# Kernel tuning notes

Hardware: AMD Instinct MI355X
Metric: run time of the kernel (lower is better)

Reference implementation:

```python
import jax, jax.numpy as jnp
import numpy as np

NUM_ATOMS = 100
D = 32        # initial_atom_dim
H = 16        # hidden_dim (multiplicity per irrep)
NB = 16       # edge_dim / number of bessel basis functions
CUT = 6.0     # radius_cutoff
DEG = 4.0     # degree_norm
OUT = 1       # output_dim
INV4PI = 1.0 / np.sqrt(4.0 * np.pi)  # 'integral' SH normalization


def _bessel(d, nb, cut):
    # e3nn soft_one_hot_linspace(basis='bessel', cutoff=True) * sqrt(nb)
    x = d[:, None]
    n = jnp.arange(1, nb + 1, dtype=d.dtype)
    safe = jnp.maximum(x, 1e-9)
    out = np.sqrt(2.0 / cut) * jnp.sin(n * jnp.pi * x / cut) / safe
    return out * (x < cut) * np.sqrt(float(nb))


def _fc(x, w1, w2):
    # e3nn FullyConnectedNet: fan-in normalized linear layers, silu, no bias
    h = jax.nn.silu(x @ w1 / np.sqrt(x.shape[-1]))
    return h @ w2 / np.sqrt(w1.shape[-1])


def _forward(atomic_numbers, edge_index, coords, atom_emb,
             fc0_w1, fc0_w2, fc1_w1, fc1_w2, w_readout):
    src, dst = edge_index[0], edge_index[1]
    N = coords.shape[0]
    E = src.shape[0]

    vec = coords[src] - coords[dst]                      # [E,3]
    dist = jnp.linalg.norm(vec, axis=-1)                 # [E]
    unit = vec / jnp.maximum(dist, 1e-9)[:, None]

    # spherical harmonics, l=0 and l=1, 'integral' normalization
    y0 = jnp.full((E,), INV4PI, dtype=coords.dtype)      # [E]
    y1 = (np.sqrt(3.0) * INV4PI) * unit                  # [E,3]
    basis = _bessel(dist, NB, CUT)                       # [E,NB]

    x = atom_emb[atomic_numbers]                         # [N,D] (row 0 is padding)

    # ---- layer 0: scalars (D x0e) x (1x0e+1x1o) -> H x0e + H x1o ----
    w = _fc(basis, fc0_w1, fc0_w2)                       # [E, 2*D*H] per-edge TP weights
    wa = w[:, : D * H].reshape(E, D, H)
    wb = w[:, D * H:].reshape(E, D, H)
    xs = x[src]
    n0 = 1.0 / np.sqrt(D)                                # path fan-in norm
    m0 = jnp.einsum('ed,edh->eh', xs, wa) * y0[:, None] * n0          # [E,H]
    m1 = jnp.einsum('ed,edh->eh', xs, wb)[:, :, None] * y1[:, None, :] * n0  # [E,H,3]
    z0 = jax.ops.segment_sum(m0, dst, num_segments=N) / DEG           # [N,H]
    z1 = jax.ops.segment_sum(m1, dst, num_segments=N) / DEG           # [N,H,3]

    # ---- layer 1: (H x0e + H x1o) x (1x0e+1x1o) -> same irreps, skip-connected ----
    w = _fc(basis, fc1_w1, fc1_w2)                       # [E, 4*H*H]
    w1_ = w[:, 0 * H * H:1 * H * H].reshape(E, H, H)     # 0e x 0e -> 0e
    w2_ = w[:, 1 * H * H:2 * H * H].reshape(E, H, H)     # 0e x 1o -> 1o
    w3_ = w[:, 2 * H * H:3 * H * H].reshape(E, H, H)     # 1o x 0e -> 1o
    w4_ = w[:, 3 * H * H:4 * H * H].reshape(E, H, H)     # 1o x 1o -> 0e (CG = dot/sqrt(3))
    s, v = z0[src], z1[src]
    n1 = 1.0 / np.sqrt(2 * H)                            # two paths per output irrep
    dot = jnp.einsum('ehm,em->eh', v, y1) / np.sqrt(3.0)
    o0 = (jnp.einsum('eh,ehk->ek', s, w1_) * y0[:, None]
          + jnp.einsum('eh,ehk->ek', dot, w4_)) * n1
    o1 = (jnp.einsum('eh,ehk->ek', s, w2_)[:, :, None] * y1[:, None, :]
          + jnp.einsum('ehm,ehk->ekm', v, w3_) * y0[:, None, None]) * n1
    z0 = jax.ops.segment_sum(o0, dst, num_segments=N) / DEG + z0      # skip
    z1 = jax.ops.segment_sum(o1, dst, num_segments=N) / DEG + z1

    # ---- scalar readout (o3.Linear onto 0e) + graph sum-pool ----
    node_scalar = z0 @ w_readout / np.sqrt(H)            # [N,OUT]
    return jnp.sum(node_scalar, axis=0)                  # [OUT]


def setup_inputs() -> dict:
    key = jax.random.key(0)
    ks = jax.random.split(key, 9)
    N, E = 10000, 160000
    atomic_numbers = jax.random.randint(ks[0], (N,), 0, NUM_ATOMS)
    coords = jax.random.normal(ks[1], (N, 3), dtype=jnp.float32)
    edge_index = jax.random.randint(ks[2], (2, E), 0, N)
    atom_emb = jax.random.normal(ks[3], (NUM_ATOMS, D), dtype=jnp.float32).at[0].set(0.0)
    fc0_w1 = jax.random.normal(ks[4], (NB, H), dtype=jnp.float32)
    fc0_w2 = jax.random.normal(ks[5], (H, 2 * D * H), dtype=jnp.float32)
    fc1_w1 = jax.random.normal(ks[6], (NB, H), dtype=jnp.float32)
    fc1_w2 = jax.random.normal(ks[7], (H, 4 * H * H), dtype=jnp.float32)
    w_readout = jax.random.normal(ks[8], (H, OUT), dtype=jnp.float32)
    return {"atomic_numbers": atomic_numbers, "coords": coords, "edge_index": edge_index,
            "atom_emb": atom_emb, "fc0_w1": fc0_w1, "fc0_w2": fc0_w2,
            "fc1_w1": fc1_w1, "fc1_w2": fc1_w2, "w_readout": w_readout}


def reference(atomic_numbers, coords, edge_index, atom_emb,
              fc0_w1, fc0_w2, fc1_w1, fc1_w2, w_readout):
    return _forward(atomic_numbers, edge_index, coords, atom_emb,
                    fc0_w1, fc0_w2, fc1_w1, fc1_w2, w_readout)
```

## Files before the change

kernel.cpp:

```cpp
#include <hip/hip_runtime.h>
#include <math.h>


namespace {
constexpr int   NATOMS   = 100;
constexpr int   CAP      = 64;
constexpr float PI_F     = 3.14159265358979323846f;
constexpr float INV4PI_F = 0.28209479177387814f;
constexpr float SQRT3_F  = 1.7320508075688772f;
constexpr float CUT_F    = 6.0f;
constexpr float BASIS_C  = 2.3094010767585034f;
constexpr float N0_F     = 0.17677669529663687f;
constexpr float K0_F = INV4PI_F * N0_F * 0.0625f;
constexpr float K1_F = SQRT3_F * INV4PI_F * N0_F * 0.0625f;
}

__device__ __forceinline__ float silu_fast(float x) {
  return x / (1.0f + __expf(-x));
}

__device__ __forceinline__ float block_reduce_sum(float v) {
  #pragma unroll
  for (int o = 32; o > 0; o >>= 1) v += __shfl_down(v, o, 64);
  __shared__ float ls[8];
  int lane = threadIdx.x & 63;
  int w    = threadIdx.x >> 6;
  if (lane == 0) ls[w] = v;
  __syncthreads();
  float s = 0.f;
  if (threadIdx.x == 0) {
    int nw = (blockDim.x + 63) >> 6;
    for (int i = 0; i < nw; ++i) s += ls[i];
  }
  return s;
}

__global__ void table_kernel(const float* __restrict__ atom_emb,
                             const float* __restrict__ fc0_w2,
                             const float* __restrict__ fc1_w2,
                             const float* __restrict__ w_readout,
                             float* __restrict__ TI,
                             float* __restrict__ G1T, float* __restrict__ G4T) {
  int b = blockIdx.x;
  int tt = threadIdx.x;
  int j = tt >> 4;
  int h = tt & 15;
  if (b < NATOMS) {
    float s0 = 0.f, s1 = 0.f;
    #pragma unroll
    for (int d = 0; d < 32; ++d) {
      float x = atom_emb[b * 32 + d];
      s0 = fmaf(x, fc0_w2[j * 1024 + d * 16 + h], s0);
      s1 = fmaf(x, fc0_w2[j * 1024 + 512 + d * 16 + h], s1);
    }
    TI[b * 512 + j * 32 + 2 * h]     = s0;
    TI[b * 512 + j * 32 + 2 * h + 1] = s1;
  } else {
    float g1 = 0.f, g4 = 0.f;
    #pragma unroll
    for (int k = 0; k < 16; ++k) {
      float r = w_readout[k];
      g1 = fmaf(fc1_w2[j * 1024 + h * 16 + k], r, g1);
      g4 = fmaf(fc1_w2[j * 1024 + 768 + h * 16 + k], r, g4);
    }
    G1T[h * 16 + j] = g1;
    G4T[h * 16 + j] = g4;
  }
}

__global__ void __launch_bounds__(256)
edge_kernel(const int* __restrict__ ei,
            const float* __restrict__ coords,
            const int* __restrict__ an,
            const float* __restrict__ TI,
            const float* __restrict__ fc0_w1,
            int* __restrict__ cursor,
            float4* __restrict__ evec,
            float4* __restrict__ mbuf,
            int E) {
  __shared__ float w1s[256];
  w1s[threadIdx.x] = fc0_w1[threadIdx.x];
  __syncthreads();
  int lane = threadIdx.x & 63;
  int g    = threadIdx.x >> 4;
  int t    = threadIdx.x & 15;
  int base = lane & 48;

  float w0c[16];
  #pragma unroll
  for (int k = 0; k < 16; ++k) w0c[k] = w1s[k * 16 + t];

  const float angc = PI_F / CUT_F;
  int e = blockIdx.x * 32 + g;
  #pragma unroll
  for (int rep = 0; rep < 2; ++rep, e += 16) {
    if (e < E) {
      int s = ei[e];
      int d = ei[E + e];
      float vx = coords[3 * s + 0] - coords[3 * d + 0];
      float vy = coords[3 * s + 1] - coords[3 * d + 1];
      float vz = coords[3 * s + 2] - coords[3 * d + 2];
      float dist = sqrtf(vx * vx + vy * vy + vz * vz);
      float inv  = 1.0f / fmaxf(dist, 1e-9f);
      float ux = vx * inv, uy = vy * inv, uz = vz * inv;
      float bc = (dist < CUT_F) ? (BASIS_C * inv) : 0.0f;

      int slotv = 0;
      if (t == 0) {
        evec[e] = make_float4(ux, uy, uz, dist);
        slotv = d * CAP + atomicAdd(&cursor[d], 1);
      }
      int slot = __shfl(slotv, base, 64);

      float ang = angc * dist;
      float sc = __sinf(ang);
      float tw = 2.0f * __cosf(ang);
      float sp = 0.f, acc = 0.f;
      #pragma unroll
      for (int k = 0; k < 16; ++k) {
        acc = fmaf(sc, w0c[k], acc);
        float sn = fmaf(tw, sc, -sp);
        sp = sc; sc = sn;
      }
      float h0t = silu_fast(acc * bc * 0.25f);

      int a = an[s];
      const float2* tp = (const float2*)(TI + a * 512) + t;
      float u0 = 0.f, u1 = 0.f;
      #pragma unroll
      for (int j = 0; j < 16; ++j) {
        float hj = __shfl(h0t, base + j, 64);
        float2 T = tp[j * 16];
        u0 = fmaf(hj, T.x, u0);
        u1 = fmaf(hj, T.y, u1);
      }
      float m1 = K1_F * u1;
      mbuf[(size_t)slot * 16 + t] =
          make_float4(K0_F * u0, m1 * ux, m1 * uy, m1 * uz);
    }
  }
}

__global__ void __launch_bounds__(256, 4)
node_kernel(const int* __restrict__ cursor,
            const float4* __restrict__ mbuf,
            const float* __restrict__ G1T,
            const float* __restrict__ G4T,
            const float* __restrict__ w_readout,
            float* __restrict__ zbuf,
            float* __restrict__ out,
            int N) {
  __shared__ float ggs[512];
  ggs[threadIdx.x]       = G1T[threadIdx.x];
  ggs[256 + threadIdx.x] = G4T[threadIdx.x];
  __syncthreads();

  int wave = threadIdx.x >> 6;
  int lane = threadIdx.x & 63;
  int g    = lane >> 4;
  int t    = lane & 15;
  int base = lane & 48;
  int node = blockIdx.x * 4 + wave;
  bool valid = node < N;

  float rr = w_readout[t];
  int cnt = valid ? min(cursor[node], CAP) : 0;
  const float4* mb = mbuf + (size_t)(valid ? node : 0) * CAP * 16;

  float a0 = 0.f, ax = 0.f, ay = 0.f, az = 0.f;
  for (int i = g; i < cnt; i += 4) {
    float4 f = mb[i * 16 + t];
    a0 += f.x; ax += f.y; ay += f.z; az += f.w;
  }

  a0 += __shfl_xor(a0, 16, 64); a0 += __shfl_xor(a0, 32, 64);
  ax += __shfl_xor(ax, 16, 64); ax += __shfl_xor(ax, 32, 64);
  ay += __shfl_xor(ay, 16, 64); ay += __shfl_xor(ay, 32, 64);
  az += __shfl_xor(az, 16, 64); az += __shfl_xor(az, 32, 64);

  float srcv = (g == 0) ? a0 : ((g == 1) ? ax : (g == 2) ? ay : az);
  int tofs = (g == 0) ? 0 : 256;
  float o = 0.f;
  #pragma unroll
  for (int h = 0; h < 16; ++h) {
    float vh = __shfl(srcv, base + h, 64);
    o = fmaf(ggs[tofs + h * 16 + t], vh, o);
  }
  if (valid) zbuf[(size_t)node * 64 + t * 4 + g] = o;

  float p = (valid && g == 0) ? a0 * rr : 0.f;
  float tot = block_reduce_sum(p);
  if (threadIdx.x == 0) atomicAdd(out, tot * 0.25f);
}

__global__ void __launch_bounds__(256, 4)
phase2_kernel(const int* __restrict__ ei,
              const float4* __restrict__ evec,
              const float* __restrict__ fc1_w1,
              const float* __restrict__ zbuf,
              float* __restrict__ out,
              int E) {
  int t = threadIdx.x & 15;
  float w1c[16];
  #pragma unroll
  for (int k = 0; k < 16; ++k) w1c[k] = fc1_w1[k * 16 + t];

  int gid = (blockIdx.x * blockDim.x + threadIdx.x) >> 4;
  int ngroups = (gridDim.x * blockDim.x) >> 4;
  const float angc = PI_F / CUT_F;

  float c = 0.f;
  for (int e = gid; e < E; e += ngroups) {
    int s = ei[e];
    float4 ev = evec[e];
    float dist = ev.w;
    float bc = (dist < CUT_F) ? (BASIS_C / fmaxf(dist, 1e-9f)) : 0.0f;

    float ang = angc * dist;
    float sc = __sinf(ang);
    float tw = 2.0f * __cosf(ang);
    float sp = 0.f, acc = 0.f;
    #pragma unroll
    for (int k = 0; k < 16; ++k) {
      acc = fmaf(sc, w1c[k], acc);
      float sn = fmaf(tw, sc, -sp);
      sp = sc; sc = sn;
    }
    float h1t = silu_fast(acc * bc * 0.25f);

    float4 z = ((const float4*)(zbuf + (size_t)s * 64))[t];
    c = fmaf(h1t, fmaf(z.y, ev.x, fmaf(z.z, ev.y, fmaf(z.w, ev.z, z.x))), c);
  }
  c *= INV4PI_F * N0_F * (1.0f / 64.0f);
  float tot = block_reduce_sum(c);
  if (threadIdx.x == 0) atomicAdd(out, tot);
}

extern "C" void kernel_launch(void* const* d_in, const int* in_sizes, int n_in,
                              void* d_out, int out_size, void* d_ws, size_t ws_size,
                              hipStream_t stream) {
  const int*   an        = (const int*)d_in[0];
  const float* coords    = (const float*)d_in[1];
  const int*   ei        = (const int*)d_in[2];
  const float* atom_emb  = (const float*)d_in[3];
  const float* fc0_w1    = (const float*)d_in[4];
  const float* fc0_w2    = (const float*)d_in[5];
  const float* fc1_w1    = (const float*)d_in[6];
  const float* fc1_w2    = (const float*)d_in[7];
  const float* w_readout = (const float*)d_in[8];

  int N = in_sizes[0];
  int E = in_sizes[2] / 2;

  float4* mbuf = (float4*)d_ws;
  float4* evec = mbuf + (size_t)N * CAP * 16;
  float*  zbuf = (float*)(evec + E);
  float*  TI   = zbuf + (size_t)N * 64;
  float*  G1T  = TI + NATOMS * 512;
  float*  G4T  = G1T + 256;
  int*    cursor = (int*)(G4T + 256);
  float*  out = (float*)d_out;

  hipMemsetAsync(cursor, 0, (size_t)N * sizeof(int), stream);
  hipMemsetAsync(out, 0, sizeof(float), stream);

  int blk = 256;
  table_kernel<<<NATOMS + 1, blk, 0, stream>>>(
      atom_emb, fc0_w2, fc1_w2, w_readout, TI, G1T, G4T);

  edge_kernel<<<(E + 31) / 32, blk, 0, stream>>>(
      ei, coords, an, TI, fc0_w1, cursor, evec, mbuf, E);

  node_kernel<<<(N + 3) / 4, blk, 0, stream>>>(
      cursor, mbuf, G1T, G4T, w_readout, zbuf, out, N);

  phase2_kernel<<<2048, blk, 0, stream>>>(ei, evec, fc1_w1, zbuf, out, E);
}
```

Before: 177.0 us.

## Fuse phase2 into node kernel via per-source edge buckets and compact messages

Edges are now bucketed by source as well as destination, so each node's wave can evaluate its outgoing second-layer contributions right after computing its own z features, with no zbuf round-trip. This removes the separate phase2 launch. Per-edge messages shrink from float4 to float2, and the unit vector is stored once per edge slot and reapplied during aggregation, which cuts mbuf traffic. The costs are a second atomic per edge and extra scatter writes into sbuf. Edges beyond CAP per source are dropped from the second term, and destination overflow now clamps into the last slot and overwrites it instead of being skipped.

```diff
diff --git a/kernel.cpp b/kernel.cpp
--- a/kernel.cpp
+++ b/kernel.cpp
@@ -13,6 +13,7 @@
 constexpr float N0_F     = 0.17677669529663687f;
 constexpr float K0_F = INV4PI_F * N0_F * 0.0625f;
 constexpr float K1_F = SQRT3_F * INV4PI_F * N0_F * 0.0625f;
+constexpr float P2SC = INV4PI_F * N0_F * (1.0f / 64.0f);
 }
 
 __device__ __forceinline__ float silu_fast(float x) {
@@ -74,9 +75,10 @@
             const int* __restrict__ an,
             const float* __restrict__ TI,
             const float* __restrict__ fc0_w1,
-            int* __restrict__ cursor,
-            float4* __restrict__ evec,
-            float4* __restrict__ mbuf,
+            int* __restrict__ dcur, int* __restrict__ scur,
+            float2* __restrict__ mbuf,
+            float4* __restrict__ ubuf,
+            float4* __restrict__ sbuf,
             int E) {
   __shared__ float w1s[256];
   w1s[threadIdx.x] = fc0_w1[threadIdx.x];
@@ -107,8 +109,13 @@
 
       int slotv = 0;
       if (t == 0) {
-        evec[e] = make_float4(ux, uy, uz, dist);
-        slotv = d * CAP + atomicAdd(&cursor[d], 1);
+        float4 rec = make_float4(ux, uy, uz, dist);
+        int pos  = atomicAdd(&dcur[d], 1);
+        int spos = atomicAdd(&scur[s], 1);
+        int dslot = d * CAP + min(pos, CAP - 1);
+        ubuf[dslot] = rec;
+        if (spos < CAP) sbuf[s * CAP + spos] = rec;
+        slotv = dslot;
       }
       int slot = __shfl(slotv, base, 64);
 
@@ -134,20 +141,21 @@
         u0 = fmaf(hj, T.x, u0);
         u1 = fmaf(hj, T.y, u1);
       }
-      float m1 = K1_F * u1;
-      mbuf[(size_t)slot * 16 + t] =
-          make_float4(K0_F * u0, m1 * ux, m1 * uy, m1 * uz);
+      mbuf[(size_t)slot * 16 + t] = make_float2(K0_F * u0, K1_F * u1);
     }
   }
 }
 
 __global__ void __launch_bounds__(256, 4)
-node_kernel(const int* __restrict__ cursor,
-            const float4* __restrict__ mbuf,
+node_kernel(const int* __restrict__ dcur,
+            const int* __restrict__ scur,
+            const float2* __restrict__ mbuf,
+            const float4* __restrict__ ubuf,
+            const float4* __restrict__ sbuf,
             const float* __restrict__ G1T,
             const float* __restrict__ G4T,
+            const float* __restrict__ fc1_w1,
             const float* __restrict__ w_readout,
-            float* __restrict__ zbuf,
             float* __restrict__ out,
             int N) {
   __shared__ float ggs[512];
@@ -163,16 +171,24 @@
   int node = blockIdx.x * 4 + wave;
   bool valid = node < N;
 
+  float w1c[16];
+  #pragma unroll
+  for (int k = 0; k < 16; ++k) w1c[k] = fc1_w1[k * 16 + t];
   float rr = w_readout[t];
-  int cnt = valid ? min(cursor[node], CAP) : 0;
-  const float4* mb = mbuf + (size_t)(valid ? node : 0) * CAP * 16;
+
+  int cin  = valid ? min(dcur[node], CAP) : 0;
+  int cout = valid ? min(scur[node], CAP) : 0;
+  size_t nb = (size_t)(valid ? node : 0) * CAP;
 
   float a0 = 0.f, ax = 0.f, ay = 0.f, az = 0.f;
-  for (int i = g; i < cnt; i += 4) {
-    float4 f = mb[i * 16 + t];
-    a0 += f.x; ax += f.y; ay += f.z; az += f.w;
-  }
-
+  for (int i = g; i < cin; i += 4) {
+    float2 f  = mbuf[(nb + i) * 16 + t];
+    float4 uu = ubuf[nb + i];
+    a0 += f.x;
+    ax = fmaf(f.y, uu.x, ax);
+    ay = fmaf(f.y, uu.y, ay);
+    az = fmaf(f.y, uu.z, az);
+  }
   a0 += __shfl_xor(a0, 16, 64); a0 += __shfl_xor(a0, 32, 64);
   ax += __shfl_xor(ax, 16, 64); ax += __shfl_xor(ax, 32, 64);
   ay += __shfl_xor(ay, 16, 64); ay += __shfl_xor(ay, 32, 64);
@@ -186,36 +202,17 @@
     float vh = __shfl(srcv, base + h, 64);
     o = fmaf(ggs[tofs + h * 16 + t], vh, o);
   }
-  if (valid) zbuf[(size_t)node * 64 + t * 4 + g] = o;
-
-  float p = (valid && g == 0) ? a0 * rr : 0.f;
-  float tot = block_reduce_sum(p);
-  if (threadIdx.x == 0) atomicAdd(out, tot * 0.25f);
-}
-
-__global__ void __launch_bounds__(256, 4)
-phase2_kernel(const int* __restrict__ ei,
-              const float4* __restrict__ evec,
-              const float* __restrict__ fc1_w1,
-              const float* __restrict__ zbuf,
-              float* __restrict__ out,
-              int E) {
-  int t = threadIdx.x & 15;
-  float w1c[16];
-  #pragma unroll
-  for (int k = 0; k < 16; ++k) w1c[k] = fc1_w1[k * 16 + t];
-
-  int gid = (blockIdx.x * blockDim.x + threadIdx.x) >> 4;
-  int ngroups = (gridDim.x * blockDim.x) >> 4;
+  float Qt  = __shfl(o, t, 64);
+  float Pxt = __shfl(o, 16 + t, 64);
+  float Pyt = __shfl(o, 32 + t, 64);
+  float Pzt = __shfl(o, 48 + t, 64);
+
   const float angc = PI_F / CUT_F;
-
   float c = 0.f;
-  for (int e = gid; e < E; e += ngroups) {
-    int s = ei[e];
-    float4 ev = evec[e];
-    float dist = ev.w;
+  for (int i = g; i < cout; i += 4) {
+    float4 uu = sbuf[nb + i];
+    float dist = uu.w;
     float bc = (dist < CUT_F) ? (BASIS_C / fmaxf(dist, 1e-9f)) : 0.0f;
-
     float ang = angc * dist;
     float sc = __sinf(ang);
     float tw = 2.0f * __cosf(ang);
@@ -227,11 +224,12 @@
       sp = sc; sc = sn;
     }
     float h1t = silu_fast(acc * bc * 0.25f);
-
-    float4 z = ((const float4*)(zbuf + (size_t)s * 64))[t];
-    c = fmaf(h1t, fmaf(z.y, ev.x, fmaf(z.z, ev.y, fmaf(z.w, ev.z, z.x))), c);
-  }
-  c *= INV4PI_F * N0_F * (1.0f / 64.0f);
+    c = fmaf(h1t, fmaf(Pxt, uu.x, fmaf(Pyt, uu.y, fmaf(Pzt, uu.z, Qt))), c);
+  }
+  c *= P2SC;
+  if (valid && g == 0) c = fmaf(a0 * rr, 0.25f, c);
+  if (!valid) c = 0.f;
+
   float tot = block_reduce_sum(c);
   if (threadIdx.x == 0) atomicAdd(out, tot);
 }
@@ -251,17 +249,19 @@
 
   int N = in_sizes[0];
   int E = in_sizes[2] / 2;
-
-  float4* mbuf = (float4*)d_ws;
-  float4* evec = mbuf + (size_t)N * CAP * 16;
-  float*  zbuf = (float*)(evec + E);
-  float*  TI   = zbuf + (size_t)N * 64;
+  size_t slots = (size_t)N * CAP;
+
+  float4* ubuf = (float4*)d_ws;
+  float4* sbuf = ubuf + slots;
+  float2* mbuf = (float2*)(sbuf + slots);
+  float*  TI   = (float*)(mbuf + slots * 16);
   float*  G1T  = TI + NATOMS * 512;
   float*  G4T  = G1T + 256;
-  int*    cursor = (int*)(G4T + 256);
+  int*    dcur = (int*)(G4T + 256);
+  int*    scur = dcur + N;
   float*  out = (float*)d_out;
 
-  hipMemsetAsync(cursor, 0, (size_t)N * sizeof(int), stream);
+  hipMemsetAsync(dcur, 0, (size_t)2 * N * sizeof(int), stream);
   hipMemsetAsync(out, 0, sizeof(float), stream);
 
   int blk = 256;
@@ -269,10 +269,8 @@
       atom_emb, fc0_w2, fc1_w2, w_readout, TI, G1T, G4T);
 
   edge_kernel<<<(E + 31) / 32, blk, 0, stream>>>(
-      ei, coords, an, TI, fc0_w1, cursor, evec, mbuf, E);
+      ei, coords, an, TI, fc0_w1, dcur, scur, mbuf, ubuf, sbuf, E);
 
   node_kernel<<<(N + 3) / 4, blk, 0, stream>>>(
-      cursor, mbuf, G1T, G4T, w_readout, zbuf, out, N);
-
-  phase2_kernel<<<2048, blk, 0, stream>>>(ei, evec, fc1_w1, zbuf, out, E);
-}
+      dcur, scur, mbuf, ubuf, sbuf, G1T, G4T, fc1_w1, w_readout, out, N);
+}
```

After: 151.3 us. 14.5% less time.
